# Kernel tuning notes

Measured on AMD Instinct MI355X. Metric: run time of the kernel, lower is better.

## Reference

```python
import jax, jax.numpy as jnp
import numpy as np

HID = 3584      # hidden_size
NQ = 16         # num query heads
NKV = 8         # num kv heads
D = 256         # head_dim
SCALE = 256.0 ** -0.5   # query_pre_attn_scalar ** -0.5
CAP = 50.0      # attn_logits_soft_cap
WINDOW = 2048   # interleaved sliding window (even layer)
THETA = 10000.0
B, S = 1, 4096


def _rope(x, positions):
    """Neox-style RoPE. x: [B,S,N,D], positions: [B,S] int."""
    half = D // 2
    inv_freq = 1.0 / (THETA ** (jnp.arange(half, dtype=jnp.float32) / half))
    freqs = positions.astype(jnp.float32)[:, :, None] * inv_freq  # [B,S,half]
    cos = jnp.cos(freqs)[:, :, None, :]  # [B,S,1,half]
    sin = jnp.sin(freqs)[:, :, None, :]
    x1, x2 = x[..., :half], x[..., half:]
    return jnp.concatenate([x1 * cos - x2 * sin, x2 * cos + x1 * sin], axis=-1)


def setup_inputs() -> dict:
    key = jax.random.key(0)
    k1, k2, k3 = jax.random.split(key, 3)
    positions = jnp.broadcast_to(jnp.arange(S, dtype=jnp.int64)[None, :], (B, S))
    hidden_states = jax.random.normal(k1, (B, S, HID), dtype=jnp.float32)
    # scale weights ~ 1/sqrt(fan_in) so activations are O(1)
    w_qkv = jax.random.normal(k2, ((NQ + 2 * NKV) * D, HID), dtype=jnp.float32) * (HID ** -0.5)
    w_o = jax.random.normal(k3, (HID, NQ * D), dtype=jnp.float32) * ((NQ * D) ** -0.5)
    return {"positions": positions, "hidden_states": hidden_states, "w_qkv": w_qkv, "w_o": w_o}


def reference(positions, hidden_states, w_qkv, w_o):
    q_size, kv_size = NQ * D, NKV * D
    qkv = jnp.einsum('bsh,oh->bso', hidden_states, w_qkv)
    q = qkv[..., :q_size].reshape(B, S, NQ, D)
    k = qkv[..., q_size:q_size + kv_size].reshape(B, S, NKV, D)
    v = qkv[..., q_size + kv_size:].reshape(B, S, NKV, D)
    q = _rope(q, positions)
    k = _rope(k, positions)
    # GQA: repeat kv heads to match query heads
    g = NQ // NKV
    k = jnp.repeat(k, g, axis=2)  # [B,S,NQ,D]
    v = jnp.repeat(v, g, axis=2)
    scores = jnp.einsum('bqhd,bkhd->bhqk', q, k) * SCALE
    # Gemma2 logit soft-capping
    scores = CAP * jnp.tanh(scores / CAP)
    i = jnp.arange(S)[:, None]
    j = jnp.arange(S)[None, :]
    mask = (j <= i) & (i - j < WINDOW)  # causal + sliding window
    scores = jnp.where(mask, scores, -1e30)
    probs = jax.nn.softmax(scores, axis=-1)
    attn = jnp.einsum('bhqk,bkhd->bqhd', probs, v).reshape(B, S, NQ * D)
    return jnp.einsum('bso,ho->bsh', attn, w_o)
```

## Files before the change

kernel.cpp:

```cpp
#include <hip/hip_runtime.h>
#include <hip/hip_bf16.h>

typedef __bf16 bf16_t;
typedef __bf16 bf16x4 __attribute__((ext_vector_type(4)));
typedef __bf16 bf16x8 __attribute__((ext_vector_type(8)));
typedef float f32x4 __attribute__((ext_vector_type(4)));

#define HIDDEN 3584
#define NQH 16
#define NKVH 8
#define DH 256
#define SEQ 4096
#define QKV_COLS 8192
#define Q_SIZE 4096
#define KV_SIZE 2048
#define WINDOW 2048
#define SCALE_F 0.0625f
#define CAP_F 50.0f

__device__ __forceinline__ void gload16(const bf16_t* g, bf16_t* l) {
  __builtin_amdgcn_global_load_lds((__attribute__((address_space(1))) void*)g,
                                   (__attribute__((address_space(3))) void*)l, 16, 0, 0);
}

__global__ __launch_bounds__(256) void cvt_f32_to_bf16(const float* __restrict__ src,
                                                       bf16_t* __restrict__ dst, long n8) {
  long i = (long)blockIdx.x * 256 + threadIdx.x;
  if (i >= n8) return;
  const float4* s4 = (const float4*)src;
  float4 a = s4[i * 2];
  float4 b = s4[i * 2 + 1];
  bf16x8 o;
  o[0] = (bf16_t)a.x; o[1] = (bf16_t)a.y; o[2] = (bf16_t)a.z; o[3] = (bf16_t)a.w;
  o[4] = (bf16_t)b.x; o[5] = (bf16_t)b.y; o[6] = (bf16_t)b.z; o[7] = (bf16_t)b.w;
  *(bf16x8*)(dst + i * 8) = o;
}

#define TILE(T, WSTR, STAGE)                                                                \
  {                                                                                         \
    char* buf = lds + ((T) & 3) * 32768;                                                    \
    bf16x8 af[8], b0, b1, b2, b3;                                                           \
    _Pragma("unroll")                                                                       \
    for (int i = 0; i < 8; ++i) af[i] = *(const bf16x8*)(buf + aoff + i * 1024);            \
    b0 = *(const bf16x8*)(buf + boff);                                                      \
    b1 = *(const bf16x8*)(buf + boff + 1024);                                               \
    if (STAGE) {                                                                            \
      char* d = lds + (((T) + 3) & 3) * 32768;                                              \
      gload16(sA0 + ((T) + 3) * 32, (bf16_t*)(d + sdst0));                                  \
      gload16(sA1 + ((T) + 3) * 32, (bf16_t*)(d + 8192 + sdst0));                           \
    }                                                                                       \
    __builtin_amdgcn_s_setprio(1);                                                          \
    _Pragma("unroll")                                                                       \
    for (int i = 0; i < 8; ++i) {                                                           \
      acc[i][0] = __builtin_amdgcn_mfma_f32_16x16x32_bf16(af[i], b0, acc[i][0], 0, 0, 0);   \
      acc[i][1] = __builtin_amdgcn_mfma_f32_16x16x32_bf16(af[i], b1, acc[i][1], 0, 0, 0);   \
    }                                                                                       \
    __builtin_amdgcn_s_setprio(0);                                                          \
    __builtin_amdgcn_s_barrier();                                                           \
    b2 = *(const bf16x8*)(buf + boff + 2048);                                               \
    b3 = *(const bf16x8*)(buf + boff + 3072);                                               \
    if (STAGE) {                                                                            \
      char* d = lds + (((T) + 3) & 3) * 32768;                                              \
      gload16(sB0 + ((T) + 3) * 32, (bf16_t*)(d + 16384 + sdst0));                          \
      gload16(sB1 + ((T) + 3) * 32, (bf16_t*)(d + 24576 + sdst0));                          \
    }                                                                                       \
    __builtin_amdgcn_s_setprio(1);                                                          \
    _Pragma("unroll")                                                                       \
    for (int i = 0; i < 8; ++i) {                                                           \
      acc[i][2] = __builtin_amdgcn_mfma_f32_16x16x32_bf16(af[i], b2, acc[i][2], 0, 0, 0);   \
      acc[i][3] = __builtin_amdgcn_mfma_f32_16x16x32_bf16(af[i], b3, acc[i][3], 0, 0, 0);   \
    }                                                                                       \
    __builtin_amdgcn_s_setprio(0);                                                          \
    asm volatile("s_waitcnt vmcnt(" WSTR ")" ::: "memory");                                 \
    __builtin_amdgcn_s_barrier();                                                           \
  }

template <int K, bool OUT_BF16>
__global__ __launch_bounds__(512, 2) void gemm_bt(const bf16_t* __restrict__ A,
                                                  const bf16_t* __restrict__ B,
                                                  void* __restrict__ Cout, int N) {
  constexpr int NT = K / 32;
  __shared__ char lds[4 * 32768];
  int tid = threadIdx.x;
  int lane = tid & 63, w = tid >> 6;
  int wm = w >> 2, wn = w & 3;
  int r16 = lane & 15, g = lane >> 4;
  int bid = blockIdx.x;
  long bm = (long)((bid & 7) * 2 + ((bid >> 3) & 1)) * 256;
  long bn = (long)(bid >> 4) * 256;
  int ro = r16 >> 1;
  int asl = ((g + ((r16 & 1) << 2)) ^ ro) << 4;
  int aoff = wm * 8192 + ro * 128 + asl;
  int boff = 16384 + wn * 4096 + ro * 128 + asl;
  int slr = lane >> 3;
  int lc = (lane & 7) ^ slr;
  int kc8 = (lc & 3) * 8;
  long mr0 = (long)(w * 8 + slr) * 2 + (lc >> 2);
  long mr1 = mr0 + 128;
  const bf16_t* sA0 = A + (bm + mr0) * K + kc8;
  const bf16_t* sA1 = A + (bm + mr1) * K + kc8;
  const bf16_t* sB0 = B + (bn + mr0) * K + kc8;
  const bf16_t* sB1 = B + (bn + mr1) * K + kc8;
  int sdst0 = w * 1024;
  f32x4 acc[8][4] = {};
#pragma unroll
  for (int u = 0; u < 3; ++u) {
    char* d = lds + u * 32768;
    gload16(sA0 + u * 32, (bf16_t*)(d + sdst0));
    gload16(sA1 + u * 32, (bf16_t*)(d + 8192 + sdst0));
    gload16(sB0 + u * 32, (bf16_t*)(d + 16384 + sdst0));
    gload16(sB1 + u * 32, (bf16_t*)(d + 24576 + sdst0));
  }
  asm volatile("s_waitcnt vmcnt(8)" ::: "memory");
  __builtin_amdgcn_s_barrier();
  int t = 0;
  for (; t < NT - 3; ++t) TILE(t, "8", true);
  TILE(t, "4", false); ++t;
  TILE(t, "0", false); ++t;
  TILE(t, "0", false);
#pragma unroll
  for (int i = 0; i < 8; ++i)
#pragma unroll
    for (int j = 0; j < 4; ++j)
#pragma unroll
      for (int r = 0; r < 4; ++r) {
        long row = bm + wm * 128 + i * 16 + g * 4 + r;
        long col = bn + wn * 64 + j * 16 + r16;
        if (OUT_BF16) ((bf16_t*)Cout)[row * N + col] = (bf16_t)acc[i][j][r];
        else          ((float*)Cout)[row * N + col]  = acc[i][j][r];
      }
}

__global__ __launch_bounds__(256) void rope_kernel(bf16_t* __restrict__ qkv) {
  long idx = (long)blockIdx.x * 256 + threadIdx.x;
  int i = (int)(idx & 127);
  long rem = idx >> 7;
  int head = (int)(rem % 24);
  int s = (int)(rem / 24);
  int base = head < NQH ? head * DH : Q_SIZE + (head - NQH) * DH;
  long p1 = (long)s * QKV_COLS + base + i;
  long p2 = p1 + 128;
  float x1 = (float)qkv[p1], x2 = (float)qkv[p2];
  float inv_freq = exp2f((float)i * -0.10381025296522976f);
  float fr = (float)s * inv_freq;
  float sn, cs;
  sincosf(fr, &sn, &cs);
  qkv[p1] = (bf16_t)(x1 * cs - x2 * sn);
  qkv[p2] = (bf16_t)(x2 * cs + x1 * sn);
}

__global__ __launch_bounds__(256) void vtrans_kernel(const bf16_t* __restrict__ qkv,
                                                     bf16_t* __restrict__ vt) {
  __shared__ bf16_t tile[64][72];
  int t = threadIdx.x;
  long s0 = (long)blockIdx.x * 64;
  long c0 = (long)blockIdx.y * 64;
#pragma unroll
  for (int it = 0; it < 2; ++it) {
    int u = t + it * 256;
    int sr = u >> 3, ch = u & 7;
    bf16x8 v = *(const bf16x8*)&qkv[(s0 + sr) * QKV_COLS + (Q_SIZE + KV_SIZE) + c0 + ch * 8];
    *(bf16x8*)&tile[sr][ch * 8] = v;
  }
  __syncthreads();
#pragma unroll
  for (int it = 0; it < 2; ++it) {
    int u = t + it * 256;
    int cr = u >> 3, ch = u & 7;
    bf16x8 o;
#pragma unroll
    for (int j = 0; j < 8; ++j) o[j] = tile[ch * 8 + j][cr];
    *(bf16x8*)&vt[(c0 + cr) * SEQ + s0 + ch * 8] = o;
  }
}

__global__ __launch_bounds__(512, 2) void attn_kernel(const bf16_t* __restrict__ qkv,
                                                      const bf16_t* __restrict__ vt,
                                                      bf16_t* __restrict__ attn_out) {
  __shared__ bf16_t Kb[2][64 * 256];
  __shared__ bf16_t Vb[2][256 * 64];
  __shared__ bf16_t Pl[8 * 1024];
  int tid = threadIdx.x;
  int lane = tid & 63, w = tid >> 6;
  int r16 = lane & 15, g = lane >> 4;
  int bid = blockIdx.x;
  int swz = (bid & 7) * 64 + (bid >> 3);
  int h = swz >> 5;
  int qb = swz & 31;
  int kvh = h >> 1;
  int qw = qb * 128 + w * 16;
  bf16x8 qf[8];
  long qoff = (long)(qw + r16) * QKV_COLS + h * DH + g * 8;
#pragma unroll
  for (int kk = 0; kk < 8; ++kk) qf[kk] = *(const bf16x8*)&qkv[qoff + kk * 32];
  f32x4 acc[16] = {};
  float lsum[4] = {};
  const bf16_t* kg = qkv + Q_SIZE + (long)kvh * DH;
  const bf16_t* vg = vt + (long)kvh * DH * SEQ;
  bf16_t* pw = Pl + w * 1024;
  int lo = qb * 128 - (WINDOW - 1);
  int t0 = lo > 0 ? (lo >> 6) : 0;
  int t1 = qb * 2 + 2;
  int qlo = qw, qhi = qw + 15;

#define ATTN_STAGE(TT)                                                                   \
  {                                                                                      \
    int b_ = (TT) & 1;                                                                   \
    int kb_ = (TT) * 64;                                                                 \
    _Pragma("unroll")                                                                    \
    for (int c = 0; c < 4; ++c) {                                                        \
      int rowk = w * 8 + c * 2 + (lane >> 5);                                            \
      gload16(kg + (long)(kb_ + rowk) * QKV_COLS + (((lane & 31) ^ (rowk & 7)) * 8),     \
              &Kb[b_][w * 2048 + c * 512]);                                              \
      int rowv = w * 32 + c * 8 + (lane >> 3);                                           \
      gload16(vg + (long)rowv * SEQ + kb_ + (((lane & 7) ^ (rowv & 7)) * 8),             \
              &Vb[b_][w * 2048 + c * 512]);                                              \
    }                                                                                    \
  }

  ATTN_STAGE(t0);
  __syncthreads();
  for (int tt = t0; tt < t1; ++tt) {
    if (tt + 1 < t1) ATTN_STAGE(tt + 1);
    int b = tt & 1;
    int kb = tt * 64;
    bool active = !(kb > qhi || kb + 63 < qlo - (WINDOW - 1));
    if (active) {
      bool full = (kb + 63 <= qlo) && (qhi - kb <= WINDOW - 1);
      f32x4 sc[4] = {};
      __builtin_amdgcn_s_setprio(1);
#pragma unroll
      for (int kk = 0; kk < 8; ++kk) {
        int sl = ((kk * 4 + g) ^ (r16 & 7)) * 8;
#pragma unroll
        for (int c = 0; c < 4; ++c) {
          bf16x8 kf = *(const bf16x8*)&Kb[b][(c * 16 + r16) * 256 + sl];
          sc[c] = __builtin_amdgcn_mfma_f32_16x16x32_bf16(qf[kk], kf, sc[c], 0, 0, 0);
        }
      }
      __builtin_amdgcn_s_setprio(0);
#pragma unroll
      for (int c = 0; c < 4; ++c)
#pragma unroll
        for (int r = 0; r < 4; ++r) {
          float s = sc[c][r];
          float e = __expf(s * (2.0f * SCALE_F / CAP_F));
          float rr = __builtin_amdgcn_rcpf(e + 1.0f);
          float p = __expf(fmaf(-100.0f, rr, 38.0f));
          if (!full) {
            int q = qw + g * 4 + r;
            int k = kb + c * 16 + r16;
            p = ((k <= q) && (q - k < WINDOW)) ? p : 0.0f;
          }
          lsum[r] += p;
          int prow = g * 4 + r;
          int pbyte = prow * 128 + ((c * 32 + r16 * 2) ^ ((prow & 7) << 4));
          *(bf16_t*)((char*)pw + pbyte) = (bf16_t)p;
        }
      bf16x8 pa[2];
#pragma unroll
      for (int pk = 0; pk < 2; ++pk) {
        int pb = r16 * 128 + ((pk * 64 + g * 16) ^ ((r16 & 7) << 4));
        pa[pk] = *(const bf16x8*)((const char*)pw + pb);
      }
      __builtin_amdgcn_s_setprio(1);
#pragma unroll
      for (int dt = 0; dt < 16; ++dt) {
        int vrow = (dt * 16 + r16) * 64;
        bf16x8 vf0 = *(const bf16x8*)&Vb[b][vrow + ((g ^ (r16 & 7)) * 8)];
        acc[dt] = __builtin_amdgcn_mfma_f32_16x16x32_bf16(pa[0], vf0, acc[dt], 0, 0, 0);
        bf16x8 vf1 = *(const bf16x8*)&Vb[b][vrow + (((4 + g) ^ (r16 & 7)) * 8)];
        acc[dt] = __builtin_amdgcn_mfma_f32_16x16x32_bf16(pa[1], vf1, acc[dt], 0, 0, 0);
      }
      __builtin_amdgcn_s_setprio(0);
    }
    __syncthreads();
  }
  float inv[4];
#pragma unroll
  for (int r = 0; r < 4; ++r) {
    float s = lsum[r];
    s += __shfl_xor(s, 1);
    s += __shfl_xor(s, 2);
    s += __shfl_xor(s, 4);
    s += __shfl_xor(s, 8);
    inv[r] = 1.0f / s;
  }
#pragma unroll
  for (int dt = 0; dt < 16; ++dt)
#pragma unroll
    for (int r = 0; r < 4; ++r) {
      long row = qw + g * 4 + r;
      attn_out[row * Q_SIZE + h * DH + dt * 16 + r16] = (bf16_t)(acc[dt][r] * inv[r]);
    }
}

extern "C" void kernel_launch(void* const* d_in, const int* in_sizes, int n_in,
                              void* d_out, int out_size, void* d_ws, size_t ws_size,
                              hipStream_t stream) {
  const float* hid_f  = (const float*)d_in[1];
  const float* wqkv_f = (const float*)d_in[2];
  const float* wo_f   = (const float*)d_in[3];
  float* out = (float*)d_out;
  char* ws = (char*)d_ws;
  bf16_t* qkv    = (bf16_t*)(ws);
  bf16_t* wo_b   = (bf16_t*)(ws + 67108864);
  bf16_t* hid_b  = (bf16_t*)(ws + 96468992);
  bf16_t* wqkv_b = (bf16_t*)(ws + 125829120);
  bf16_t* attn_b = (bf16_t*)(ws + 96468992);
  bf16_t* vt     = (bf16_t*)(ws + 130023424);

  cvt_f32_to_bf16<<<7168, 256, 0, stream>>>(hid_f, hid_b, 14680064 / 8);
  cvt_f32_to_bf16<<<14336, 256, 0, stream>>>(wqkv_f, wqkv_b, 29360128 / 8);
  cvt_f32_to_bf16<<<7168, 256, 0, stream>>>(wo_f, wo_b, 14680064 / 8);
  gemm_bt<HIDDEN, true><<<512, 512, 0, stream>>>(hid_b, wqkv_b, qkv, QKV_COLS);
  rope_kernel<<<49152, 256, 0, stream>>>(qkv);
  vtrans_kernel<<<dim3(64, 32), 256, 0, stream>>>(qkv, vt);
  attn_kernel<<<512, 512, 0, stream>>>(qkv, vt, attn_b);
  gemm_bt<Q_SIZE, false><<<224, 512, 0, stream>>>(attn_b, wo_b, out, HIDDEN);
}
```

Before: 607.1 us.

## Single-buffer attention K/V tiles for higher occupancy, vectorize RoPE, use exp2

The attention kernel drops double-buffered K/V shared tiles in favour of a single buffer loaded and synchronised at each iteration, cutting LDS use so more blocks can reside per CU, and raises the launch-bounds occupancy hint. This gives up the prefetch overlap and may force register spilling given the large accumulator array. The softcap exponentials are rewritten with exp2 and folded constants, and RoPE now processes eight elements per thread with vector loads and stores.

```diff
diff --git a/kernel.cpp b/kernel.cpp
--- a/kernel.cpp
+++ b/kernel.cpp
@@ -133,20 +133,27 @@
 
 __global__ __launch_bounds__(256) void rope_kernel(bf16_t* __restrict__ qkv) {
   long idx = (long)blockIdx.x * 256 + threadIdx.x;
-  int i = (int)(idx & 127);
-  long rem = idx >> 7;
+  int i8 = (int)(idx & 15) * 8;
+  long rem = idx >> 4;
   int head = (int)(rem % 24);
   int s = (int)(rem / 24);
   int base = head < NQH ? head * DH : Q_SIZE + (head - NQH) * DH;
-  long p1 = (long)s * QKV_COLS + base + i;
-  long p2 = p1 + 128;
-  float x1 = (float)qkv[p1], x2 = (float)qkv[p2];
-  float inv_freq = exp2f((float)i * -0.10381025296522976f);
-  float fr = (float)s * inv_freq;
-  float sn, cs;
-  sincosf(fr, &sn, &cs);
-  qkv[p1] = (bf16_t)(x1 * cs - x2 * sn);
-  qkv[p2] = (bf16_t)(x2 * cs + x1 * sn);
+  long p1 = (long)s * QKV_COLS + base + i8;
+  bf16x8 x1 = *(const bf16x8*)&qkv[p1];
+  bf16x8 x2 = *(const bf16x8*)&qkv[p1 + 128];
+  bf16x8 o1, o2;
+#pragma unroll
+  for (int j = 0; j < 8; ++j) {
+    float inv_freq = exp2f((float)(i8 + j) * -0.10381025296522976f);
+    float fr = (float)s * inv_freq;
+    float sn, cs;
+    sincosf(fr, &sn, &cs);
+    float a = (float)x1[j], b = (float)x2[j];
+    o1[j] = (bf16_t)(a * cs - b * sn);
+    o2[j] = (bf16_t)(b * cs + a * sn);
+  }
+  *(bf16x8*)&qkv[p1] = o1;
+  *(bf16x8*)&qkv[p1 + 128] = o2;
 }
 
 __global__ __launch_bounds__(256) void vtrans_kernel(const bf16_t* __restrict__ qkv,
@@ -174,11 +181,11 @@
   }
 }
 
-__global__ __launch_bounds__(512, 2) void attn_kernel(const bf16_t* __restrict__ qkv,
+__global__ __launch_bounds__(512, 4) void attn_kernel(const bf16_t* __restrict__ qkv,
                                                       const bf16_t* __restrict__ vt,
                                                       bf16_t* __restrict__ attn_out) {
-  __shared__ bf16_t Kb[2][64 * 256];
-  __shared__ bf16_t Vb[2][256 * 64];
+  __shared__ bf16_t Kb[64 * 256];
+  __shared__ bf16_t Vb[256 * 64];
   __shared__ bf16_t Pl[8 * 1024];
   int tid = threadIdx.x;
   int lane = tid & 63, w = tid >> 6;
@@ -202,28 +209,18 @@
   int t0 = lo > 0 ? (lo >> 6) : 0;
   int t1 = qb * 2 + 2;
   int qlo = qw, qhi = qw + 15;
-
-#define ATTN_STAGE(TT)                                                                   \
-  {                                                                                      \
-    int b_ = (TT) & 1;                                                                   \
-    int kb_ = (TT) * 64;                                                                 \
-    _Pragma("unroll")                                                                    \
-    for (int c = 0; c < 4; ++c) {                                                        \
-      int rowk = w * 8 + c * 2 + (lane >> 5);                                            \
-      gload16(kg + (long)(kb_ + rowk) * QKV_COLS + (((lane & 31) ^ (rowk & 7)) * 8),     \
-              &Kb[b_][w * 2048 + c * 512]);                                              \
-      int rowv = w * 32 + c * 8 + (lane >> 3);                                           \
-      gload16(vg + (long)rowv * SEQ + kb_ + (((lane & 7) ^ (rowv & 7)) * 8),             \
-              &Vb[b_][w * 2048 + c * 512]);                                              \
-    }                                                                                    \
-  }
-
-  ATTN_STAGE(t0);
-  __syncthreads();
   for (int tt = t0; tt < t1; ++tt) {
-    if (tt + 1 < t1) ATTN_STAGE(tt + 1);
-    int b = tt & 1;
     int kb = tt * 64;
+#pragma unroll
+    for (int c = 0; c < 4; ++c) {
+      int rowk = w * 8 + c * 2 + (lane >> 5);
+      gload16(kg + (long)(kb + rowk) * QKV_COLS + (((lane & 31) ^ (rowk & 7)) * 8),
+              &Kb[w * 2048 + c * 512]);
+      int rowv = w * 32 + c * 8 + (lane >> 3);
+      gload16(vg + (long)rowv * SEQ + kb + (((lane & 7) ^ (rowv & 7)) * 8),
+              &Vb[w * 2048 + c * 512]);
+    }
+    __syncthreads();
     bool active = !(kb > qhi || kb + 63 < qlo - (WINDOW - 1));
     if (active) {
       bool full = (kb + 63 <= qlo) && (qhi - kb <= WINDOW - 1);
@@ -234,19 +231,22 @@
         int sl = ((kk * 4 + g) ^ (r16 & 7)) * 8;
 #pragma unroll
         for (int c = 0; c < 4; ++c) {
-          bf16x8 kf = *(const bf16x8*)&Kb[b][(c * 16 + r16) * 256 + sl];
+          bf16x8 kf = *(const bf16x8*)&Kb[(c * 16 + r16) * 256 + sl];
           sc[c] = __builtin_amdgcn_mfma_f32_16x16x32_bf16(qf[kk], kf, sc[c], 0, 0, 0);
         }
       }
       __builtin_amdgcn_s_setprio(0);
+      const float C1 = 0.0036067376022224085f;
+      const float C2 = 144.26950408889634f;
+      const float C3 = 54.82241191667733f;
 #pragma unroll
       for (int c = 0; c < 4; ++c)
 #pragma unroll
         for (int r = 0; r < 4; ++r) {
           float s = sc[c][r];
-          float e = __expf(s * (2.0f * SCALE_F / CAP_F));
+          float e = exp2f(s * C1);
           float rr = __builtin_amdgcn_rcpf(e + 1.0f);
-          float p = __expf(fmaf(-100.0f, rr, 38.0f));
+          float p = exp2f(fmaf(-C2, rr, C3));
           if (!full) {
             int q = qw + g * 4 + r;
             int k = kb + c * 16 + r16;
@@ -267,9 +267,9 @@
 #pragma unroll
       for (int dt = 0; dt < 16; ++dt) {
         int vrow = (dt * 16 + r16) * 64;
-        bf16x8 vf0 = *(const bf16x8*)&Vb[b][vrow + ((g ^ (r16 & 7)) * 8)];
+        bf16x8 vf0 = *(const bf16x8*)&Vb[vrow + ((g ^ (r16 & 7)) * 8)];
         acc[dt] = __builtin_amdgcn_mfma_f32_16x16x32_bf16(pa[0], vf0, acc[dt], 0, 0, 0);
-        bf16x8 vf1 = *(const bf16x8*)&Vb[b][vrow + (((4 + g) ^ (r16 & 7)) * 8)];
+        bf16x8 vf1 = *(const bf16x8*)&Vb[vrow + (((4 + g) ^ (r16 & 7)) * 8)];
         acc[dt] = __builtin_amdgcn_mfma_f32_16x16x32_bf16(pa[1], vf1, acc[dt], 0, 0, 0);
       }
       __builtin_amdgcn_s_setprio(0);
@@ -314,7 +314,7 @@
   cvt_f32_to_bf16<<<14336, 256, 0, stream>>>(wqkv_f, wqkv_b, 29360128 / 8);
   cvt_f32_to_bf16<<<7168, 256, 0, stream>>>(wo_f, wo_b, 14680064 / 8);
   gemm_bt<HIDDEN, true><<<512, 512, 0, stream>>>(hid_b, wqkv_b, qkv, QKV_COLS);
-  rope_kernel<<<49152, 256, 0, stream>>>(qkv);
+  rope_kernel<<<6144, 256, 0, stream>>>(qkv);
   vtrans_kernel<<<dim3(64, 32), 256, 0, stream>>>(qkv, vt);
   attn_kernel<<<512, 512, 0, stream>>>(qkv, vt, attn_b);
   gemm_bt<Q_SIZE, false><<<224, 512, 0, stream>>>(attn_b, wo_b, out, HIDDEN);
```

New measurement: 862.3 us. 42.0% more time.

## Fuse Q RoPE into attention, vectorize K RoPE, reverse q-block order for odd heads

Applied to the files above, without the earlier changes.

RoPE for query heads now runs inside the attention kernel on the Q fragments held in registers, so the standalone pass only rotates K heads, using 8-wide vector loads and stores per thread. This removes one global read and write of Q. Odd heads also process query blocks in reverse order, which balances causal and sliding-window work across concurrently scheduled blocks. The cost is extra sincos math in the attention kernel prologue and more register pressure there.

```diff
diff --git a/kernel.cpp b/kernel.cpp
--- a/kernel.cpp
+++ b/kernel.cpp
@@ -131,22 +131,28 @@
       }
 }
 
-__global__ __launch_bounds__(256) void rope_kernel(bf16_t* __restrict__ qkv) {
+__global__ __launch_bounds__(256) void rope_k_kernel(bf16_t* __restrict__ qkv) {
   long idx = (long)blockIdx.x * 256 + threadIdx.x;
-  int i = (int)(idx & 127);
-  long rem = idx >> 7;
-  int head = (int)(rem % 24);
-  int s = (int)(rem / 24);
-  int base = head < NQH ? head * DH : Q_SIZE + (head - NQH) * DH;
-  long p1 = (long)s * QKV_COLS + base + i;
-  long p2 = p1 + 128;
-  float x1 = (float)qkv[p1], x2 = (float)qkv[p2];
-  float inv_freq = exp2f((float)i * -0.10381025296522976f);
-  float fr = (float)s * inv_freq;
-  float sn, cs;
-  sincosf(fr, &sn, &cs);
-  qkv[p1] = (bf16_t)(x1 * cs - x2 * sn);
-  qkv[p2] = (bf16_t)(x2 * cs + x1 * sn);
+  int i8 = (int)(idx & 15) * 8;
+  long rem = idx >> 4;
+  int head = (int)(rem & 7);
+  int s = (int)(rem >> 3);
+  long p1 = (long)s * QKV_COLS + Q_SIZE + head * DH + i8;
+  bf16x8 x1 = *(const bf16x8*)&qkv[p1];
+  bf16x8 x2 = *(const bf16x8*)&qkv[p1 + 128];
+  bf16x8 o1, o2;
+#pragma unroll
+  for (int j = 0; j < 8; ++j) {
+    float inv_freq = exp2f((float)(i8 + j) * -0.10381025296522976f);
+    float fr = (float)s * inv_freq;
+    float sn, cs;
+    sincosf(fr, &sn, &cs);
+    float a = (float)x1[j], b = (float)x2[j];
+    o1[j] = (bf16_t)(a * cs - b * sn);
+    o2[j] = (bf16_t)(b * cs + a * sn);
+  }
+  *(bf16x8*)&qkv[p1] = o1;
+  *(bf16x8*)&qkv[p1 + 128] = o2;
 }
 
 __global__ __launch_bounds__(256) void vtrans_kernel(const bf16_t* __restrict__ qkv,
@@ -186,13 +192,27 @@
   int bid = blockIdx.x;
   int swz = (bid & 7) * 64 + (bid >> 3);
   int h = swz >> 5;
-  int qb = swz & 31;
+  int qb0 = swz & 31;
+  int qb = (h & 1) ? (31 - qb0) : qb0;
   int kvh = h >> 1;
   int qw = qb * 128 + w * 16;
   bf16x8 qf[8];
   long qoff = (long)(qw + r16) * QKV_COLS + h * DH + g * 8;
 #pragma unroll
   for (int kk = 0; kk < 8; ++kk) qf[kk] = *(const bf16x8*)&qkv[qoff + kk * 32];
+#pragma unroll
+  for (int kk = 0; kk < 4; ++kk)
+#pragma unroll
+    for (int j = 0; j < 8; ++j) {
+      int d = kk * 32 + g * 8 + j;
+      float inv_freq = exp2f((float)d * -0.10381025296522976f);
+      float fr = (float)(qw + r16) * inv_freq;
+      float sn, cs;
+      sincosf(fr, &sn, &cs);
+      float a = (float)qf[kk][j], b2 = (float)qf[kk + 4][j];
+      qf[kk][j] = (bf16_t)(a * cs - b2 * sn);
+      qf[kk + 4][j] = (bf16_t)(b2 * cs + a * sn);
+    }
   f32x4 acc[16] = {};
   float lsum[4] = {};
   const bf16_t* kg = qkv + Q_SIZE + (long)kvh * DH;
@@ -314,7 +334,7 @@
   cvt_f32_to_bf16<<<14336, 256, 0, stream>>>(wqkv_f, wqkv_b, 29360128 / 8);
   cvt_f32_to_bf16<<<7168, 256, 0, stream>>>(wo_f, wo_b, 14680064 / 8);
   gemm_bt<HIDDEN, true><<<512, 512, 0, stream>>>(hid_b, wqkv_b, qkv, QKV_COLS);
-  rope_kernel<<<49152, 256, 0, stream>>>(qkv);
+  rope_k_kernel<<<2048, 256, 0, stream>>>(qkv);
   vtrans_kernel<<<dim3(64, 32), 256, 0, stream>>>(qkv, vt);
   attn_kernel<<<512, 512, 0, stream>>>(qkv, vt, attn_b);
   gemm_bt<Q_SIZE, false><<<224, 512, 0, stream>>>(attn_b, wo_b, out, HIDDEN);
```

Measured after the change: 585.8 us. -3.5%, faster.
